# Kernel optimization log

Measured on AMD Instinct MI355X. Metric: run time of the kernel, lower is better.

The kernel has to match this reference:

```python
import jax, jax.numpy as jnp
import numpy as np

N, D_IN, D_H, C, E, K = 10000, 512, 256, 40, 160000, 16
ETA = 0.5
EPS = 1e-8


def _lin_init(key, out_dim, in_dim, bias):
    s = 1.0 / np.sqrt(in_dim)
    kw, kb = jax.random.split(key)
    W = jax.random.uniform(kw, (out_dim, in_dim), jnp.float32, -s, s)
    if bias:
        b = jax.random.uniform(kb, (out_dim,), jnp.float32, -s, s)
        return W, b
    return W


def setup_inputs() -> dict:
    key = jax.random.key(0)
    ks = jax.random.split(key, 8)
    x = jax.random.normal(ks[0], (N, D_IN), jnp.float32)
    edge_index = jax.random.randint(ks[1], (2, E), 0, N, jnp.int32).astype(jnp.int64)
    y = jax.random.randint(ks[2], (N,), 0, C, jnp.int32).astype(jnp.int64)
    mask = jax.random.uniform(ks[3], (N, N), jnp.float32)
    W1_l, b1 = _lin_init(ks[4], D_H, D_IN, True)   # SAGEConv lin_l (aggregated neighbors, with bias)
    W1_r = _lin_init(ks[5], D_H, D_IN, False)       # SAGEConv lin_r (root, no bias)
    W2_l, b2 = _lin_init(ks[6], C, D_H, True)
    W2_r = _lin_init(ks[7], C, D_H, False)
    return dict(x=x, edge_index=edge_index, y=y, mask=mask,
                W1_l=W1_l, b1=b1, W1_r=W1_r, W2_l=W2_l, b2=b2, W2_r=W2_r)


def _sage_conv(x, src, dst, W_l, b_l, W_r, n):
    # mean aggregation of source features onto destinations
    agg_sum = jax.ops.segment_sum(x[src], dst, num_segments=n)           # [N, F]
    cnt = jax.ops.segment_sum(jnp.ones((src.shape[0], 1), x.dtype), dst, num_segments=n)
    agg = agg_sum / jnp.maximum(cnt, 1.0)
    return agg @ W_l.T + b_l + x @ W_r.T


def _label_fusion(emb, y, mask):
    # cosine similarity matrix (sim_matrix) -> mask -> topk -> exp-weighted one-hot label fusion
    nrm = jnp.maximum(jnp.linalg.norm(emb, axis=1, keepdims=True), EPS)
    en = emb / nrm
    sim = (en @ en.T) * mask                                             # [N, N]
    vals, idx = jax.lax.top_k(sim, K)                                    # [N, K]
    fetch_sim = jnp.exp(vals)                                            # [N, K]
    one_hot = jax.nn.one_hot(y, C, dtype=emb.dtype)                      # [N, C]
    fetch_label = one_hot[idx]                                           # [N, K, C]
    return jnp.einsum('nk,nkc->nc', fetch_sim, fetch_label)              # [N, C]


def reference(x, edge_index, y, mask, W1_l, b1, W1_r, W2_l, b2, W2_r):
    src, dst = edge_index[0], edge_index[1]
    n = x.shape[0]
    h = jax.nn.elu(_sage_conv(x, src, dst, W1_l, b1, W1_r, n))           # embedding [N, D_H]
    lc = jax.nn.elu(_sage_conv(h, src, dst, W2_l, b2, W2_r, n))          # [N, C]
    p_lc = jax.nn.log_softmax(lc, axis=1)
    # similarity branch is computed under torch.no_grad in the original
    fused = jax.lax.stop_gradient(_label_fusion(h, y, mask))
    p_sim = jax.nn.log_softmax(fused, axis=1)
    out = ETA * p_lc + (1.0 - ETA) * p_sim
    return out, h
```

## Files before the change

kernel.cpp:

```cpp
#include <hip/hip_runtime.h>
#include <math.h>

#define N_NODES 10000
#define D_IN    512
#define D_H     256
#define NCLS    40
#define NEDGE   160000
#define KTOP    16
#define NFRAG   625
#define CSPL    13
#define ROWS    64
#define RT      157
#define SLOTS   6
#define LSTREAM 52
#define CPR     (LSTREAM * SLOTS)
#define RESC    32

typedef __attribute__((ext_vector_type(8))) short bf16x8;
typedef __attribute__((ext_vector_type(4))) float f32x4;

__device__ __forceinline__ void gload_lds16(const void* g, void* l) {
    __builtin_amdgcn_global_load_lds(
        (const __attribute__((address_space(1))) void*)g,
        (__attribute__((address_space(3))) void*)l, 16, 0, 0);
}

__global__ void transpose_kernel(const float* __restrict__ W1_l, const float* __restrict__ W1_r,
                                 const float* __restrict__ W2_l, const float* __restrict__ W2_r,
                                 float* __restrict__ W1lT, float* __restrict__ W1rT,
                                 float* __restrict__ W2lT, float* __restrict__ W2rT) {
    int i = blockIdx.x * 256 + threadIdx.x;
    if (i < D_H * D_IN) {
        int r = i / D_IN, c = i % D_IN;
        W1lT[(size_t)c * D_H + r] = W1_l[i];
        W1rT[(size_t)c * D_H + r] = W1_r[i];
    }
    if (i < NCLS * D_H) {
        int r = i / D_H, c = i % D_H;
        W2lT[(size_t)c * NCLS + r] = W2_l[i];
        W2rT[(size_t)c * NCLS + r] = W2_r[i];
    }
}

__global__ void count_kernel(const int* __restrict__ dst, int* __restrict__ cnt) {
    int e = blockIdx.x * 256 + threadIdx.x;
    if (e < NEDGE) {
        int d = dst[e];
        d = (d >= 0 && d < N_NODES) ? d : 0;
        atomicAdd(&cnt[d], 1);
    }
}

__global__ void prefix_kernel(const int* __restrict__ cnt, int* __restrict__ rowptr,
                              int* __restrict__ cursor) {
    __shared__ int sp[256];
    int t = threadIdx.x;
    int b0 = t * 40;
    int e0 = (b0 + 40 < N_NODES) ? b0 + 40 : N_NODES;
    int s = 0;
    for (int i = b0; i < e0; i++) s += cnt[i];
    sp[t] = s;
    __syncthreads();
    for (int o = 1; o < 256; o <<= 1) {
        int add = (t >= o) ? sp[t - o] : 0;
        __syncthreads();
        sp[t] += add;
        __syncthreads();
    }
    int run = sp[t] - s;
    for (int i = b0; i < e0; i++) {
        rowptr[i] = run; cursor[i] = run; run += cnt[i];
    }
    if (t == 255) rowptr[N_NODES] = run;
}

__global__ void bucket_kernel(const int* __restrict__ src, const int* __restrict__ dst,
                              int* __restrict__ cursor, int* __restrict__ nbr) {
    int e = blockIdx.x * 256 + threadIdx.x;
    if (e < NEDGE) {
        int d = dst[e];
        d = (d >= 0 && d < N_NODES) ? d : 0;
        int p = atomicAdd(&cursor[d], 1);
        if (p >= 0 && p < NEDGE) {
            int s = src[e];
            nbr[p] = (s >= 0 && s < N_NODES) ? s : 0;
        }
    }
}

__global__ __launch_bounds__(256) void proj1_kernel(const float* __restrict__ x,
        const float* __restrict__ W1lT, const float* __restrict__ W1rT,
        float* __restrict__ xw1, float* __restrict__ xwr) {
    __shared__ float sx[8][D_IN];
    int tid = threadIdx.x;
    int nb0 = blockIdx.x * 8;
    #pragma unroll
    for (int u = 0; u < 4; u++) {
        int s = tid + u * 256;
        int nb = s >> 7;
        int c4 = (s & 127) << 2;
        int n = nb0 + nb;
        float4 v = make_float4(0.f, 0.f, 0.f, 0.f);
        if (n < N_NODES) v = *(const float4*)&x[(size_t)n * D_IN + c4];
        *(float4*)&sx[nb][c4] = v;
    }
    __syncthreads();
    int j = tid;
    float accl[8] = {0,0,0,0,0,0,0,0};
    float accr[8] = {0,0,0,0,0,0,0,0};
    for (int i = 0; i < D_IN; i += 4) {
        float wl0 = W1lT[(size_t)(i + 0) * D_H + j];
        float wl1 = W1lT[(size_t)(i + 1) * D_H + j];
        float wl2 = W1lT[(size_t)(i + 2) * D_H + j];
        float wl3 = W1lT[(size_t)(i + 3) * D_H + j];
        float wr0 = W1rT[(size_t)(i + 0) * D_H + j];
        float wr1 = W1rT[(size_t)(i + 1) * D_H + j];
        float wr2 = W1rT[(size_t)(i + 2) * D_H + j];
        float wr3 = W1rT[(size_t)(i + 3) * D_H + j];
        #pragma unroll
        for (int nb = 0; nb < 8; nb++) {
            float4 xx = *(const float4*)&sx[nb][i];
            float tl = accl[nb], tr = accr[nb];
            tl = fmaf(xx.x, wl0, tl); tl = fmaf(xx.y, wl1, tl);
            tl = fmaf(xx.z, wl2, tl); tl = fmaf(xx.w, wl3, tl);
            tr = fmaf(xx.x, wr0, tr); tr = fmaf(xx.y, wr1, tr);
            tr = fmaf(xx.z, wr2, tr); tr = fmaf(xx.w, wr3, tr);
            accl[nb] = tl; accr[nb] = tr;
        }
    }
    for (int nb = 0; nb < 8; nb++) {
        int n = nb0 + nb;
        if (n < N_NODES) {
            xw1[(size_t)n * D_H + j] = accl[nb];
            xwr[(size_t)n * D_H + j] = accr[nb];
        }
    }
}

__global__ __launch_bounds__(256) void gather_h_fused_kernel(const float* __restrict__ xw1,
        const float* __restrict__ xwr, const int* __restrict__ nbr,
        const int* __restrict__ rowptr, const int* __restrict__ cnt,
        const float* __restrict__ b1, const float* __restrict__ W2lT,
        const float* __restrict__ W2rT, float* __restrict__ h, float* __restrict__ en,
        unsigned short* __restrict__ enb, float* __restrict__ outh,
        float* __restrict__ hwl, float* __restrict__ hwr) {
    __shared__ float sh[4][D_H];
    int wid = threadIdx.x >> 6, lane = threadIdx.x & 63;
    int n = blockIdx.x * 4 + wid;
    if (n >= N_NODES) return;
    int st = rowptr[n], deg = cnt[n];
    float a[4] = {0,0,0,0};
    for (int j = 0; j < deg; j++) {
        int s = nbr[st + j];
        float4 v = *(const float4*)&xw1[(size_t)s * D_H + lane * 4];
        a[0] += v.x; a[1] += v.y; a[2] += v.z; a[3] += v.w;
    }
    float inv = 1.0f / fmaxf((float)deg, 1.0f);
    float4 r4 = *(const float4*)&xwr[(size_t)n * D_H + lane * 4];
    float4 bb = *(const float4*)&b1[lane * 4];
    float o0 = a[0] * inv + bb.x + r4.x;
    float o1 = a[1] * inv + bb.y + r4.y;
    float o2 = a[2] * inv + bb.z + r4.z;
    float o3 = a[3] * inv + bb.w + r4.w;
    o0 = o0 > 0.f ? o0 : expm1f(o0);
    o1 = o1 > 0.f ? o1 : expm1f(o1);
    o2 = o2 > 0.f ? o2 : expm1f(o2);
    o3 = o3 > 0.f ? o3 : expm1f(o3);
    float4 hv = make_float4(o0, o1, o2, o3);
    *(float4*)&h[(size_t)n * D_H + lane * 4] = hv;
    *(float4*)&outh[(size_t)n * D_H + lane * 4] = hv;
    *(float4*)&sh[wid][lane * 4] = hv;

    float ss = o0 * o0 + o1 * o1 + o2 * o2 + o3 * o3;
    for (int o = 32; o; o >>= 1) ss += __shfl_xor(ss, o);
    float ninv = 1.0f / fmaxf(sqrtf(ss), 1e-8f);
    float e[4] = {o0 * ninv, o1 * ninv, o2 * ninv, o3 * ninv};
    *(float4*)&en[(size_t)n * D_H + lane * 4] = make_float4(e[0], e[1], e[2], e[3]);
    unsigned int p[4];
    #pragma unroll
    for (int k = 0; k < 4; k++) {
        unsigned int ub = __float_as_uint(e[k]);
        p[k] = (ub + 0x7FFFu + ((ub >> 16) & 1u)) >> 16;
    }
    uint2 packed = make_uint2(p[0] | (p[1] << 16), p[2] | (p[3] << 16));
    *(uint2*)&enb[(size_t)n * D_H + lane * 4] = packed;

    if (lane < NCLS) {
        float al = 0.f, ar = 0.f;
        for (int i = 0; i < D_H; i++) {
            float hvv = sh[wid][i];
            al = fmaf(hvv, W2lT[(size_t)i * NCLS + lane], al);
            ar = fmaf(hvv, W2rT[(size_t)i * NCLS + lane], ar);
        }
        hwl[(size_t)n * NCLS + lane] = al;
        hwr[(size_t)n * NCLS + lane] = ar;
    }
}

__global__ void gather_lc_kernel(const float* __restrict__ hwl, const float* __restrict__ hwr,
                                 const int* __restrict__ nbr, const int* __restrict__ rowptr,
                                 const int* __restrict__ cnt, const float* __restrict__ b2,
                                 float* __restrict__ lcls) {
    int wid = threadIdx.x >> 6, lane = threadIdx.x & 63;
    int n = blockIdx.x * 4 + wid;
    if (n >= N_NODES) return;
    int st = rowptr[n], deg = cnt[n];
    float a = 0.f;
    if (lane < NCLS) {
        for (int j = 0; j < deg; j++) {
            int s = nbr[st + j];
            a += hwl[(size_t)s * NCLS + lane];
        }
    }
    float inv = 1.0f / fmaxf((float)deg, 1.0f);
    float v;
    if (lane < NCLS) {
        v = a * inv + b2[lane] + hwr[(size_t)n * NCLS + lane];
        v = v > 0.f ? v : expm1f(v);
    } else {
        v = -INFINITY;
    }
    float m = v;
    for (int o = 32; o; o >>= 1) m = fmaxf(m, __shfl_xor(m, o));
    float ex = (lane < NCLS) ? expf(v - m) : 0.0f;
    float s = ex;
    for (int o = 32; o; o >>= 1) s += __shfl_xor(s, o);
    if (lane < NCLS) lcls[(size_t)n * NCLS + lane] = v - m - logf(s);
}

__global__ __launch_bounds__(256) void sim_topk_kernel(const unsigned short* __restrict__ enb,
        const float* __restrict__ mask, float* __restrict__ pv, int* __restrict__ pi) {
    __shared__ __align__(16) char Abuf[2][8192];

    int rt = blockIdx.x / CSPL, cs = blockIdx.x % CSPL;
    int tid = threadIdx.x;
    int w = tid >> 6, l = tid & 63;
    int l15 = l & 15, lh = l >> 4;
    int r = rt * ROWS + w * 16 + l15;
    int rc = (r < N_NODES) ? r : (N_NODES - 1);

    int fbeg = cs * 48 + (cs ? 1 : 0);
    int fend = fbeg + (cs ? 48 : 49);

    bf16x8 bfr[8];
    const unsigned short* brow = enb + (size_t)rc * D_H + 8 * lh;
    #pragma unroll
    for (int ks = 0; ks < 8; ks++) bfr[ks] = *(const bf16x8*)(brow + ks * 32);

    float tv[SLOTS]; int ti[SLOTS];
    #pragma unroll
    for (int k = 0; k < SLOTS; k++) { tv[k] = -INFINITY; ti[k] = 0; }

    const float* mrow = mask + (size_t)rc * N_NODES;

    int swz = (l15 & 7) << 4;
    const char* rb0[8];
    const char* rb1[8];
    {
        const char* base0 = &Abuf[0][l15 * 512];
        const char* base1 = &Abuf[1][l15 * 512];
        #pragma unroll
        for (int ks = 0; ks < 8; ks++) {
            int off = (lh * 16 + ks * 64) ^ swz;
            rb0[ks] = base0 + off;
            rb1[ks] = base1 + off;
        }
    }

    int row0 = 4 * w + (l >> 5);
    int row1 = row0 + 2;
    int tcol = l & 31;
    int g0 = tcol ^ (row0 & 7);
    int g1 = tcol ^ (row1 & 7);
    const char* gB = (const char*)enb;

    gload_lds16(gB + (((size_t)(fbeg * 16 + row0)) << 9) + g0 * 16, &Abuf[0][w * 2048]);
    gload_lds16(gB + (((size_t)(fbeg * 16 + row1)) << 9) + g1 * 16, &Abuf[0][w * 2048 + 1024]);
    __syncthreads();

    float4 mm = *(const float4*)&mrow[fbeg * 16 + lh * 4];
    int cur = 0;
    for (int f = fbeg; f < fend; ++f) {
        int fn = f + 1;
        bool hasNext = (fn < fend);

        float4 mmn = make_float4(0.f, 0.f, 0.f, 0.f);
        if (hasNext) {
            gload_lds16(gB + (((size_t)(fn * 16 + row0)) << 9) + g0 * 16, &Abuf[cur ^ 1][w * 2048]);
            gload_lds16(gB + (((size_t)(fn * 16 + row1)) << 9) + g1 * 16, &Abuf[cur ^ 1][w * 2048 + 1024]);
            mmn = *(const float4*)&mrow[fn * 16 + lh * 4];
        }

        f32x4 acc = {0.f, 0.f, 0.f, 0.f};
        if (cur == 0) {
            #pragma unroll
            for (int ks = 0; ks < 8; ks++) {
                bf16x8 af = *(const bf16x8*)rb0[ks];
                acc = __builtin_amdgcn_mfma_f32_16x16x32_bf16(af, bfr[ks], acc, 0, 0, 0);
            }
        } else {
            #pragma unroll
            for (int ks = 0; ks < 8; ks++) {
                bf16x8 af = *(const bf16x8*)rb1[ks];
                acc = __builtin_amdgcn_mfma_f32_16x16x32_bf16(af, bfr[ks], acc, 0, 0, 0);
            }
        }

        int c0 = f * 16 + lh * 4;
        float vv[4];
        vv[0] = acc[0] * mm.x; vv[1] = acc[1] * mm.y;
        vv[2] = acc[2] * mm.z; vv[3] = acc[3] * mm.w;
        #pragma unroll
        for (int j = 0; j < 4; j++) {
            float v = vv[j]; int c = c0 + j;
            bool hh[SLOTS];
            #pragma unroll
            for (int k = 0; k < SLOTS; k++) hh[k] = tv[k] < v;
            float nv[SLOTS]; int ni[SLOTS];
            #pragma unroll
            for (int k = 0; k < SLOTS - 1; k++) {
                nv[k] = hh[k + 1] ? tv[k + 1] : (hh[k] ? v : tv[k]);
                ni[k] = hh[k + 1] ? ti[k + 1] : (hh[k] ? c : ti[k]);
            }
            nv[SLOTS - 1] = hh[SLOTS - 1] ? v : tv[SLOTS - 1];
            ni[SLOTS - 1] = hh[SLOTS - 1] ? c : ti[SLOTS - 1];
            #pragma unroll
            for (int k = 0; k < SLOTS; k++) { tv[k] = nv[k]; ti[k] = ni[k]; }
        }

        __syncthreads();
        cur ^= 1;
        mm = mmn;
    }

    if (r < N_NODES) {
        int stream = cs * 4 + lh;
        float* pvp = pv + (size_t)r * CPR + stream;
        int*   pip = pi + (size_t)r * CPR + stream;
        #pragma unroll
        for (int k = 0; k < SLOTS; k++) { pvp[k * LSTREAM] = tv[k]; pip[k * LSTREAM] = ti[k]; }
    }
}

__global__ __launch_bounds__(256) void rescore_merge_kernel(const float* __restrict__ en,
        const float* __restrict__ mask, const float* __restrict__ pv, const int* __restrict__ pi,
        const int* __restrict__ y, const float* __restrict__ lcls, float* __restrict__ out) {
    __shared__ float sen[4][D_H];
    int wid = threadIdx.x >> 6, lane = threadIdx.x & 63;
    int r = blockIdx.x * 4 + wid;
    if (r >= N_NODES) return;
    *(float4*)&sen[wid][lane * 4] = *(const float4*)&en[(size_t)r * D_H + lane * 4];

    float v0 = -INFINITY, v1 = -INFINITY, v2 = -INFINITY;
    float v3 = -INFINITY, v4 = -INFINITY, v5 = -INFINITY;
    int   i0 = 0x7FFFFFFF, i1 = 0x7FFFFFFF, i2 = 0x7FFFFFFF;
    int   i3 = 0x7FFFFFFF, i4 = 0x7FFFFFFF, i5 = 0x7FFFFFFF;
    if (lane < LSTREAM) {
        const float* pvr = pv + (size_t)r * CPR + lane;
        const int*   pir = pi + (size_t)r * CPR + lane;
        v0 = pvr[0*LSTREAM]; v1 = pvr[1*LSTREAM]; v2 = pvr[2*LSTREAM];
        v3 = pvr[3*LSTREAM]; v4 = pvr[4*LSTREAM]; v5 = pvr[5*LSTREAM];
        i0 = pir[0*LSTREAM]; i1 = pir[1*LSTREAM]; i2 = pir[2*LSTREAM];
        i3 = pir[3*LSTREAM]; i4 = pir[4*LSTREAM]; i5 = pir[5*LSTREAM];
    }
    int p = SLOTS - 1;
    int my_cand = 0;
    #pragma unroll 1
    for (int t = 0; t < RESC; t++) {
        float cur  = (p < 0) ? -INFINITY :
                     (p == 5 ? v5 : p == 4 ? v4 : p == 3 ? v3 : p == 2 ? v2 : p == 1 ? v1 : v0);
        int   curi = (p < 0) ? 0x7FFFFFFF :
                     (p == 5 ? i5 : p == 4 ? i4 : p == 3 ? i3 : p == 2 ? i2 : p == 1 ? i1 : i0);
        float rv = cur; int ri = curi;
        #pragma unroll
        for (int o = 1; o < 64; o <<= 1) {
            float ov = __shfl_xor(rv, o); int oi = __shfl_xor(ri, o);
            bool bet = (ov > rv) || (ov == rv && oi < ri);
            rv = bet ? ov : rv; ri = bet ? oi : ri;
        }
        if (curi == ri && p >= 0) p--;
        if (lane == t) my_cand = ri;
    }
    int cand = __shfl(my_cand, lane & 31);
    cand = (cand >= 0 && cand < N_NODES) ? cand : 0;

    __syncthreads();

    int half = lane >> 5;
    const float* erow = &en[(size_t)cand * D_H + half * 128];
    const float* srow = &sen[wid][half * 128];
    float dot = 0.0f;
    #pragma unroll 8
    for (int k = 0; k < 128; k += 4) {
        float4 e = *(const float4*)&erow[k];
        dot = fmaf(srow[k + 0], e.x, dot);
        dot = fmaf(srow[k + 1], e.y, dot);
        dot = fmaf(srow[k + 2], e.z, dot);
        dot = fmaf(srow[k + 3], e.w, dot);
    }
    dot += __shfl_xor(dot, 32);
    float cv = (lane < RESC) ? dot * mask[(size_t)r * N_NODES + cand] : -INFINITY;

    float fc = 0.0f;
    #pragma unroll 1
    for (int t = 0; t < KTOP; t++) {
        float rv = cv; int ri = (lane < RESC) ? cand : 0x7FFFFFFF;
        #pragma unroll
        for (int o = 1; o < 64; o <<= 1) {
            float ov = __shfl_xor(rv, o); int oi = __shfl_xor(ri, o);
            bool bet = (ov > rv) || (ov == rv && oi < ri);
            rv = bet ? ov : rv; ri = bet ? oi : ri;
        }
        if (lane < RESC && cand == ri) cv = -INFINITY;
        int ris = (ri >= 0 && ri < N_NODES) ? ri : 0;
        int lbl = y[ris];
        if (lane == lbl) fc += expf(rv);
    }
    float fval = (lane < NCLS) ? fc : -INFINITY;
    float m = fval;
    for (int o = 32; o; o >>= 1) m = fmaxf(m, __shfl_xor(m, o));
    float ex = (lane < NCLS) ? expf(fval - m) : 0.0f;
    float s = ex;
    for (int o = 32; o; o >>= 1) s += __shfl_xor(s, o);
    if (lane < NCLS)
        out[(size_t)r * NCLS + lane] = 0.5f * lcls[(size_t)r * NCLS + lane]
                                     + 0.5f * (fval - m - logf(s));
}

extern "C" void kernel_launch(void* const* d_in, const int* in_sizes, int n_in,
                              void* d_out, int out_size, void* d_ws, size_t ws_size,
                              hipStream_t stream) {
    const float* x    = (const float*)d_in[0];
    const int*   ei   = (const int*)  d_in[1];
    const int*   y    = (const int*)  d_in[2];
    const float* mask = (const float*)d_in[3];
    const float* W1_l = (const float*)d_in[4];
    const float* b1   = (const float*)d_in[5];
    const float* W1_r = (const float*)d_in[6];
    const float* W2_l = (const float*)d_in[7];
    const float* b2   = (const float*)d_in[8];
    const float* W2_r = (const float*)d_in[9];

    float* out   = (float*)d_out;
    float* out_h = out + (size_t)N_NODES * NCLS;

    int*   cnt    = (int*)d_ws;
    int*   rowptr = cnt + 10240;
    int*   cursor = rowptr + 10304;
    int*   nbr    = cursor + 10240;
    float* xw1    = (float*)(nbr + 160256);
    float* xwr    = xw1 + (size_t)N_NODES * D_H;
    float* h      = xwr + (size_t)N_NODES * D_H;
    float* en     = h   + (size_t)N_NODES * D_H;
    unsigned short* enb = (unsigned short*)(en + (size_t)N_NODES * D_H);
    float* lcls   = (float*)(enb + (size_t)N_NODES * D_H);
    float* hwl    = lcls + (size_t)N_NODES * NCLS;
    float* hwr    = hwl + (size_t)N_NODES * NCLS;
    float* W1lT   = hwr + (size_t)N_NODES * NCLS;
    float* W1rT   = W1lT + (size_t)D_IN * D_H;
    float* W2lT   = W1rT + (size_t)D_IN * D_H;
    float* W2rT   = W2lT + (size_t)D_H * NCLS;
    float* pv     = xw1;
    int*   pi     = (int*)(W2rT + (size_t)D_H * NCLS);

    const int* src = ei;
    const int* dst = ei + NEDGE;

    hipMemsetAsync(cnt, 0, 10240 * sizeof(int), stream);

    transpose_kernel<<<(D_H * D_IN + 255) / 256, 256, 0, stream>>>(
        W1_l, W1_r, W2_l, W2_r, W1lT, W1rT, W2lT, W2rT);
    count_kernel<<<(NEDGE + 255) / 256, 256, 0, stream>>>(dst, cnt);
    prefix_kernel<<<1, 256, 0, stream>>>(cnt, rowptr, cursor);
    bucket_kernel<<<(NEDGE + 255) / 256, 256, 0, stream>>>(src, dst, cursor, nbr);
    proj1_kernel<<<(N_NODES + 7) / 8, 256, 0, stream>>>(x, W1lT, W1rT, xw1, xwr);
    gather_h_fused_kernel<<<(N_NODES + 3) / 4, 256, 0, stream>>>(
        xw1, xwr, nbr, rowptr, cnt, b1, W2lT, W2rT, h, en, enb, out_h, hwl, hwr);
    gather_lc_kernel<<<(N_NODES + 3) / 4, 256, 0, stream>>>(hwl, hwr, nbr, rowptr, cnt, b2, lcls);
    sim_topk_kernel<<<RT * CSPL, 256, 0, stream>>>(enb, mask, pv, pi);
    rescore_merge_kernel<<<(N_NODES + 3) / 4, 256, 0, stream>>>(en, mask, pv, pi, y, lcls, out);
}
```

Before: 509.1 us.

## Triple-buffer LDS tiles in sim_topk with two-deep prefetch and manual vmcnt waits

```diff
diff --git a/kernel.cpp b/kernel.cpp
--- a/kernel.cpp
+++ b/kernel.cpp
@@ -230,7 +230,7 @@
 
 __global__ __launch_bounds__(256) void sim_topk_kernel(const unsigned short* __restrict__ enb,
         const float* __restrict__ mask, float* __restrict__ pv, int* __restrict__ pi) {
-    __shared__ __align__(16) char Abuf[2][8192];
+    __shared__ __align__(16) char Abuf[3][8192];
 
     int rt = blockIdx.x / CSPL, cs = blockIdx.x % CSPL;
     int tid = threadIdx.x;
@@ -253,18 +253,11 @@
 
     const float* mrow = mask + (size_t)rc * N_NODES;
 
-    int swz = (l15 & 7) << 4;
-    const char* rb0[8];
-    const char* rb1[8];
+    int offs[8];
     {
-        const char* base0 = &Abuf[0][l15 * 512];
-        const char* base1 = &Abuf[1][l15 * 512];
-        #pragma unroll
-        for (int ks = 0; ks < 8; ks++) {
-            int off = (lh * 16 + ks * 64) ^ swz;
-            rb0[ks] = base0 + off;
-            rb1[ks] = base1 + off;
-        }
+        int swz = (l15 & 7) << 4;
+        #pragma unroll
+        for (int ks = 0; ks < 8; ks++) offs[ks] = (lh * 16 + ks * 64) ^ swz;
     }
 
     int row0 = 4 * w + (l >> 5);
@@ -273,37 +266,37 @@
     int g0 = tcol ^ (row0 & 7);
     int g1 = tcol ^ (row1 & 7);
     const char* gB = (const char*)enb;
-
-    gload_lds16(gB + (((size_t)(fbeg * 16 + row0)) << 9) + g0 * 16, &Abuf[0][w * 2048]);
-    gload_lds16(gB + (((size_t)(fbeg * 16 + row1)) << 9) + g1 * 16, &Abuf[0][w * 2048 + 1024]);
-    __syncthreads();
-
-    float4 mm = *(const float4*)&mrow[fbeg * 16 + lh * 4];
+    char* lds0 = &Abuf[0][0];
+
+    gload_lds16(gB + (((size_t)(fbeg * 16 + row0)) << 9) + g0 * 16, lds0 + w * 2048);
+    gload_lds16(gB + (((size_t)(fbeg * 16 + row1)) << 9) + g1 * 16, lds0 + w * 2048 + 1024);
+    gload_lds16(gB + (((size_t)((fbeg + 1) * 16 + row0)) << 9) + g0 * 16, lds0 + 8192 + w * 2048);
+    gload_lds16(gB + (((size_t)((fbeg + 1) * 16 + row1)) << 9) + g1 * 16, lds0 + 8192 + w * 2048 + 1024);
+
+    float4 mm  = *(const float4*)&mrow[fbeg * 16 + lh * 4];
+    float4 mm1 = *(const float4*)&mrow[(fbeg + 1) * 16 + lh * 4];
+
     int cur = 0;
     for (int f = fbeg; f < fend; ++f) {
-        int fn = f + 1;
-        bool hasNext = (fn < fend);
-
-        float4 mmn = make_float4(0.f, 0.f, 0.f, 0.f);
-        if (hasNext) {
-            gload_lds16(gB + (((size_t)(fn * 16 + row0)) << 9) + g0 * 16, &Abuf[cur ^ 1][w * 2048]);
-            gload_lds16(gB + (((size_t)(fn * 16 + row1)) << 9) + g1 * 16, &Abuf[cur ^ 1][w * 2048 + 1024]);
-            mmn = *(const float4*)&mrow[fn * 16 + lh * 4];
-        }
-
+        bool more = (f + 1 < fend);
+        if (more) asm volatile("s_waitcnt vmcnt(2)" ::: "memory");
+        else      asm volatile("s_waitcnt vmcnt(0)" ::: "memory");
+        __builtin_amdgcn_s_barrier();
+        __builtin_amdgcn_sched_barrier(0);
+        float4 mm2 = make_float4(0.f, 0.f, 0.f, 0.f);
+        if (f + 2 < fend) {
+            int nb = cur + 2; nb = (nb >= 3) ? nb - 3 : nb;
+            char* dst = lds0 + nb * 8192 + w * 2048;
+            gload_lds16(gB + (((size_t)((f + 2) * 16 + row0)) << 9) + g0 * 16, dst);
+            gload_lds16(gB + (((size_t)((f + 2) * 16 + row1)) << 9) + g1 * 16, dst + 1024);
+            mm2 = *(const float4*)&mrow[(f + 2) * 16 + lh * 4];
+        }
+        const char* lbase = lds0 + cur * 8192 + l15 * 512;
         f32x4 acc = {0.f, 0.f, 0.f, 0.f};
-        if (cur == 0) {
-            #pragma unroll
-            for (int ks = 0; ks < 8; ks++) {
-                bf16x8 af = *(const bf16x8*)rb0[ks];
-                acc = __builtin_amdgcn_mfma_f32_16x16x32_bf16(af, bfr[ks], acc, 0, 0, 0);
-            }
-        } else {
-            #pragma unroll
-            for (int ks = 0; ks < 8; ks++) {
-                bf16x8 af = *(const bf16x8*)rb1[ks];
-                acc = __builtin_amdgcn_mfma_f32_16x16x32_bf16(af, bfr[ks], acc, 0, 0, 0);
-            }
+        #pragma unroll
+        for (int ks = 0; ks < 8; ks++) {
+            bf16x8 af = *(const bf16x8*)(lbase + offs[ks]);
+            acc = __builtin_amdgcn_mfma_f32_16x16x32_bf16(af, bfr[ks], acc, 0, 0, 0);
         }
 
         int c0 = f * 16 + lh * 4;
@@ -328,9 +321,8 @@
             for (int k = 0; k < SLOTS; k++) { tv[k] = nv[k]; ti[k] = ni[k]; }
         }
 
-        __syncthreads();
-        cur ^= 1;
-        mm = mmn;
+        mm = mm1; mm1 = mm2;
+        cur = (cur == 2) ? 0 : cur + 1;
     }
 
     if (r < N_NODES) {
```

Result: no change. 502.1 us (-1.4%).
